# Optimization experiments

Hardware: AMD Instinct MI355X
Metric: run time of the kernel (lower is better)

The kernel has to match this reference:

```python
import jax, jax.numpy as jnp
import numpy as np

B, T, I, U, O, BB = 256, 1024, 64, 256, 64, 128  # batch, seq, input, units, output, backbone_units

def lecun_tanh(x):
    return 1.7159 * jnp.tanh(0.666 * x)

def setup_inputs() -> dict:
    key = jax.random.key(0)
    ks = jax.random.split(key, 13)
    def lin(k, fan_in, fan_out):
        bound = 1.0 / np.sqrt(fan_in)
        kw, kb = jax.random.split(k)
        W = jax.random.uniform(kw, (fan_in, fan_out), jnp.float32, -bound, bound)
        b = jax.random.uniform(kb, (fan_out,), jnp.float32, -bound, bound)
        return W, b
    x = jax.random.normal(ks[0], (B, T, I), jnp.float32)
    W_bb, b_bb = lin(ks[1], I + U, BB)   # backbone Linear
    W_ff1, b_ff1 = lin(ks[2], BB, U)
    W_ff2, b_ff2 = lin(ks[3], BB, U)
    W_ta, b_ta = lin(ks[4], BB, U)       # time_a
    W_tb, b_tb = lin(ks[5], BB, U)       # time_b
    W_fc, b_fc = lin(ks[6], U, O)        # readout
    return {"x": x, "W_bb": W_bb, "b_bb": b_bb, "W_ff1": W_ff1, "b_ff1": b_ff1,
            "W_ff2": W_ff2, "b_ff2": b_ff2, "W_ta": W_ta, "b_ta": b_ta,
            "W_tb": W_tb, "b_tb": b_tb, "W_fc": W_fc, "b_fc": b_fc}

def reference(x, W_bb, b_bb, W_ff1, b_ff1, W_ff2, b_ff2, W_ta, b_ta, W_tb, b_tb, W_fc, b_fc):
    ts = jnp.float32(1.0)  # default elapsed time per step
    def step(h, xt):
        z = jnp.concatenate([xt, h], axis=-1)          # [B, I+U]
        g = lecun_tanh(z @ W_bb + b_bb)                # [B, BB]
        ff1 = jnp.tanh(g @ W_ff1 + b_ff1)              # [B, U]
        ff2 = jnp.tanh(g @ W_ff2 + b_ff2)
        t_interp = jax.nn.sigmoid((g @ W_ta + b_ta) * ts + (g @ W_tb + b_tb))
        h_new = ff1 * (1.0 - t_interp) + t_interp * ff2
        return h_new, h_new
    h0 = jnp.zeros((x.shape[0], U), x.dtype)
    h_last, hs = jax.lax.scan(step, h0, jnp.swapaxes(x, 0, 1))  # hs: [T, B, U]
    hs = jnp.swapaxes(hs, 0, 1)                                  # [B, T, U]
    out = hs @ W_fc + b_fc                                       # [B, T, O]
    return out, h_last
```

## Files before the change

kernel.cpp:

```cpp
#include <hip/hip_runtime.h>
#include <stdint.h>

#define B_ 256
#define T_ 1024
#define I_ 64
#define U_ 256
#define O_ 64
#define BB_ 128

typedef unsigned int u32;
typedef unsigned short u16;
typedef _Float16 half2_t __attribute__((ext_vector_type(2)));

#if defined(__has_builtin)
#if __has_builtin(__builtin_amdgcn_fdot2)
#define USE_DOT2 1
#else
#define USE_DOT2 0
#endif
#else
#define USE_DOT2 0
#endif

static __device__ __forceinline__ u32 packpair(float a, float b) {
  half2_t h; h.x = (_Float16)a; h.y = (_Float16)b;
  return __builtin_bit_cast(u32, h);
}
static __device__ __forceinline__ float unpack_lo(u32 u) {
  half2_t h = __builtin_bit_cast(half2_t, u); return (float)h.x;
}
static __device__ __forceinline__ float unpack_hi(u32 u) {
  half2_t h = __builtin_bit_cast(half2_t, u); return (float)h.y;
}
static __device__ __forceinline__ float dot2acc(u32 w, u32 z, float acc) {
#if USE_DOT2
  return __builtin_amdgcn_fdot2(__builtin_bit_cast(half2_t, w),
                                __builtin_bit_cast(half2_t, z), acc, false);
#else
  half2_t hw = __builtin_bit_cast(half2_t, w);
  half2_t hz = __builtin_bit_cast(half2_t, z);
  acc += (float)hw.x * (float)hz.x;
  acc += (float)hw.y * (float)hz.y;
  return acc;
#endif
}

template <int CTRL>
static __device__ __forceinline__ float dpp_mov_f(float v) {
  return __builtin_bit_cast(float, __builtin_amdgcn_update_dpp(
      0, __builtin_bit_cast(int, v), CTRL, 0xF, 0xF, true));
}
#define DPP_XOR1 0xB1
#define DPP_XOR2 0x4E
#define DPP_HMIR 0x141
#define DPP_MIRR 0x140

static __device__ __forceinline__ float fast_tanh(float x) {
  return 1.0f - 2.0f / (1.0f + __expf(2.0f * x));
}
static __device__ __forceinline__ float fast_sigmoid(float x) {
  return 1.0f / (1.0f + __expf(-x));
}

template <bool DEFER>
__global__ __launch_bounds__(1024)
void cfc_kernel(const float* __restrict__ x,
                const float* __restrict__ W_bb, const float* __restrict__ b_bb,
                const float* __restrict__ W_ff1, const float* __restrict__ b_ff1,
                const float* __restrict__ W_ff2, const float* __restrict__ b_ff2,
                const float* __restrict__ W_ta,  const float* __restrict__ b_ta,
                const float* __restrict__ W_tb,  const float* __restrict__ b_tb,
                const float* __restrict__ W_fc,  const float* __restrict__ b_fc,
                float* __restrict__ out, u32* __restrict__ Hbuf)
{
  __shared__ __align__(16) u32 s_z2[160];
  __shared__ __align__(16) u32 s_g2[64];
  u16* s_gh = (u16*)s_g2;

  const int tid = threadIdx.x;
  const int r   = blockIdx.x;

  const int ca  = tid >> 3;
  const int kga = tid & 7;
  const int jb = tid >> 2;
  const int kq = tid & 3;
  const int ro = tid >> 4;
  const int rk = tid & 15;

  u32 wbb[20];
#pragma unroll
  for (int j = 0; j < 5; ++j)
#pragma unroll
    for (int q = 0; q < 4; ++q) {
      int p = 4 * (kga + 8 * j) + q;
      wbb[4 * j + q] = packpair(W_bb[(2 * p) * BB_ + ca],
                                W_bb[(2 * p + 1) * BB_ + ca]);
    }
  u32 wf1[16], wf2[16], wta[16], wtb[16];
#pragma unroll
  for (int j = 0; j < 4; ++j)
#pragma unroll
    for (int q = 0; q < 4; ++q) {
      int p = 4 * (kq + 4 * j) + q;
      int k0 = 2 * p, k1 = 2 * p + 1;
      wf1[4 * j + q] = packpair(W_ff1[k0 * U_ + jb], W_ff1[k1 * U_ + jb]);
      wf2[4 * j + q] = packpair(W_ff2[k0 * U_ + jb], W_ff2[k1 * U_ + jb]);
      wta[4 * j + q] = packpair(W_ta [k0 * U_ + jb], W_ta [k1 * U_ + jb]);
      wtb[4 * j + q] = packpair(W_tb [k0 * U_ + jb], W_tb [k1 * U_ + jb]);
    }
  u32 wfc[8];
  float bfo = 0.f;
  if (!DEFER) {
#pragma unroll
    for (int j = 0; j < 2; ++j)
#pragma unroll
      for (int q = 0; q < 4; ++q) {
        int p = 4 * (rk + 16 * j) + q;
        wfc[4 * j + q] = packpair(W_fc[(2 * p) * O_ + ro],
                                  W_fc[(2 * p + 1) * O_ + ro]);
      }
    bfo = b_fc[ro];
  }
  const float bbbc = b_bb[ca];
  const float b1 = b_ff1[jb], b2 = b_ff2[jb];
  const float bta = b_ta[jb], btb = b_tb[jb];

  const float* xrow = x + (size_t)r * T_ * I_;
  const size_t out_row = (size_t)r * T_ * O_;
  u32* __restrict__ hrow = DEFER ? (Hbuf + (size_t)r * T_ * (U_ / 2)) : nullptr;

  if (tid < 160) s_z2[tid] = 0u;
  __syncthreads();
  if (tid < 32) {
    float2 xv = ((const float2*)xrow)[tid];
    s_z2[tid] = packpair(xv.x, xv.y);
  }
  __syncthreads();

  for (int t = 0; t < T_; ++t) {
    float2 xv;
    const bool ldx = (tid < 32) && (t + 1 < T_);
    if (ldx) xv = ((const float2*)(xrow + (size_t)(t + 1) * I_))[tid];

    float bacc = 0.f;
#pragma unroll
    for (int j = 0; j < 5; ++j) {
      uint4 zz = *reinterpret_cast<const uint4*>(s_z2 + 4 * (kga + 8 * j));
      bacc = dot2acc(wbb[4 * j + 0], zz.x, bacc);
      bacc = dot2acc(wbb[4 * j + 1], zz.y, bacc);
      bacc = dot2acc(wbb[4 * j + 2], zz.z, bacc);
      bacc = dot2acc(wbb[4 * j + 3], zz.w, bacc);
    }
    bacc += dpp_mov_f<DPP_XOR1>(bacc);
    bacc += dpp_mov_f<DPP_XOR2>(bacc);
    bacc += dpp_mov_f<DPP_HMIR>(bacc);
    float g = 1.7159f * fast_tanh(0.666f * (bacc + bbbc));

    float racc = 0.f;
    if (!DEFER) {
#pragma unroll
      for (int j = 0; j < 2; ++j) {
        uint4 hh = *reinterpret_cast<const uint4*>(s_z2 + 32 + 4 * (rk + 16 * j));
        racc = dot2acc(wfc[4 * j + 0], hh.x, racc);
        racc = dot2acc(wfc[4 * j + 1], hh.y, racc);
        racc = dot2acc(wfc[4 * j + 2], hh.z, racc);
        racc = dot2acc(wfc[4 * j + 3], hh.w, racc);
      }
      racc += dpp_mov_f<DPP_XOR1>(racc);
      racc += dpp_mov_f<DPP_XOR2>(racc);
      racc += dpp_mov_f<DPP_HMIR>(racc);
      racc += dpp_mov_f<DPP_MIRR>(racc);
    }
    if ((tid & 7) == 0)
      s_gh[ca] = __builtin_bit_cast(u16, (_Float16)g);
    if (!DEFER && t > 0 && rk == 0)
      out[out_row + (size_t)(t - 1) * O_ + ro] = racc + bfo;
    __syncthreads();

    float a1 = 0.f, a2 = 0.f, a3 = 0.f, a4 = 0.f;
#pragma unroll
    for (int j = 0; j < 4; ++j) {
      uint4 gg = *reinterpret_cast<const uint4*>(s_g2 + 4 * (kq + 4 * j));
      a1 = dot2acc(wf1[4 * j + 0], gg.x, a1);
      a1 = dot2acc(wf1[4 * j + 1], gg.y, a1);
      a1 = dot2acc(wf1[4 * j + 2], gg.z, a1);
      a1 = dot2acc(wf1[4 * j + 3], gg.w, a1);
      a2 = dot2acc(wf2[4 * j + 0], gg.x, a2);
      a2 = dot2acc(wf2[4 * j + 1], gg.y, a2);
      a2 = dot2acc(wf2[4 * j + 2], gg.z, a2);
      a2 = dot2acc(wf2[4 * j + 3], gg.w, a2);
      a3 = dot2acc(wta[4 * j + 0], gg.x, a3);
      a3 = dot2acc(wta[4 * j + 1], gg.y, a3);
      a3 = dot2acc(wta[4 * j + 2], gg.z, a3);
      a3 = dot2acc(wta[4 * j + 3], gg.w, a3);
      a4 = dot2acc(wtb[4 * j + 0], gg.x, a4);
      a4 = dot2acc(wtb[4 * j + 1], gg.y, a4);
      a4 = dot2acc(wtb[4 * j + 2], gg.z, a4);
      a4 = dot2acc(wtb[4 * j + 3], gg.w, a4);
    }
    a1 += dpp_mov_f<DPP_XOR1>(a1); a1 += dpp_mov_f<DPP_XOR2>(a1);
    a2 += dpp_mov_f<DPP_XOR1>(a2); a2 += dpp_mov_f<DPP_XOR2>(a2);
    a3 += dpp_mov_f<DPP_XOR1>(a3); a3 += dpp_mov_f<DPP_XOR2>(a3);
    a4 += dpp_mov_f<DPP_XOR1>(a4); a4 += dpp_mov_f<DPP_XOR2>(a4);
    float f1 = fast_tanh(a1 + b1);
    float f2 = fast_tanh(a2 + b2);
    float ti = fast_sigmoid(a3 + bta + a4 + btb);
    float h  = f1 + ti * (f2 - f1);
    float hq = dpp_mov_f<DPP_HMIR>(h);

    if ((tid & 7) == 0) {
      u32 pr = packpair(h, hq);
      int m = tid >> 3;
      s_z2[32 + m] = pr;
      if (DEFER) hrow[(size_t)t * (U_ / 2) + m] = pr;
    }
    if (ldx) s_z2[tid] = packpair(xv.x, xv.y);
    __syncthreads();
  }

  if (!DEFER) {
    float racc = 0.f;
#pragma unroll
    for (int j = 0; j < 2; ++j) {
      uint4 hh = *reinterpret_cast<const uint4*>(s_z2 + 32 + 4 * (rk + 16 * j));
      racc = dot2acc(wfc[4 * j + 0], hh.x, racc);
      racc = dot2acc(wfc[4 * j + 1], hh.y, racc);
      racc = dot2acc(wfc[4 * j + 2], hh.z, racc);
      racc = dot2acc(wfc[4 * j + 3], hh.w, racc);
    }
    racc += dpp_mov_f<DPP_XOR1>(racc);
    racc += dpp_mov_f<DPP_XOR2>(racc);
    racc += dpp_mov_f<DPP_HMIR>(racc);
    racc += dpp_mov_f<DPP_MIRR>(racc);
    if (rk == 0)
      out[out_row + (size_t)(T_ - 1) * O_ + ro] = racc + bfo;
  }

  if (tid < 128) {
    u32 hp = s_z2[32 + tid];
    float2 hv; hv.x = unpack_lo(hp); hv.y = unpack_hi(hp);
    ((float2*)(out + (size_t)B_ * T_ * O_))[r * 128 + tid] = hv;
  }
}

__global__ __launch_bounds__(512)
void ro_kernel(const u32* __restrict__ Hbuf,
               const float* __restrict__ W_fc, const float* __restrict__ b_fc,
               float* __restrict__ out)
{
  __shared__ __align__(16) u32 s_h[8 * 128];
  const int tid = threadIdx.x;
  const int o   = tid & 63;
  const int w   = tid >> 6;
  const int r   = blockIdx.x;

  u32 wfc[128];
#pragma unroll
  for (int p = 0; p < 128; ++p)
    wfc[p] = packpair(W_fc[(2 * p) * O_ + o], W_fc[(2 * p + 1) * O_ + o]);
  const float bo = b_fc[o];

  const u32* hrow = Hbuf + (size_t)r * T_ * 128;
  const size_t out_row = (size_t)r * T_ * O_;

  for (int c = 0; c < T_ / 8; ++c) {
    *(uint2*)(s_h + 2 * tid) =
        *(const uint2*)(hrow + (size_t)c * 1024 + 2 * tid);
    __syncthreads();
    float acc = bo;
    const uint4* h4 = reinterpret_cast<const uint4*>(s_h + w * 128);
#pragma unroll
    for (int i = 0; i < 32; ++i) {
      uint4 hh = h4[i];
      acc = dot2acc(wfc[4 * i + 0], hh.x, acc);
      acc = dot2acc(wfc[4 * i + 1], hh.y, acc);
      acc = dot2acc(wfc[4 * i + 2], hh.z, acc);
      acc = dot2acc(wfc[4 * i + 3], hh.w, acc);
    }
    out[out_row + (size_t)(8 * c + w) * O_ + o] = acc;
    __syncthreads();
  }
}

extern "C" void kernel_launch(void* const* d_in, const int* in_sizes, int n_in,
                              void* d_out, int out_size, void* d_ws, size_t ws_size,
                              hipStream_t stream) {
  const float* x     = (const float*)d_in[0];
  const float* W_bb  = (const float*)d_in[1];
  const float* b_bb  = (const float*)d_in[2];
  const float* W_ff1 = (const float*)d_in[3];
  const float* b_ff1 = (const float*)d_in[4];
  const float* W_ff2 = (const float*)d_in[5];
  const float* b_ff2 = (const float*)d_in[6];
  const float* W_ta  = (const float*)d_in[7];
  const float* b_ta  = (const float*)d_in[8];
  const float* W_tb  = (const float*)d_in[9];
  const float* b_tb  = (const float*)d_in[10];
  const float* W_fc  = (const float*)d_in[11];
  const float* b_fc  = (const float*)d_in[12];
  float* out = (float*)d_out;

  const size_t h_bytes = (size_t)B_ * T_ * (U_ / 2) * sizeof(u32);
  if (ws_size >= h_bytes) {
    u32* Hbuf = (u32*)d_ws;
    cfc_kernel<true><<<dim3(B_), dim3(1024), 0, stream>>>(
        x, W_bb, b_bb, W_ff1, b_ff1, W_ff2, b_ff2,
        W_ta, b_ta, W_tb, b_tb, W_fc, b_fc, out, Hbuf);
    ro_kernel<<<dim3(B_), dim3(512), 0, stream>>>(Hbuf, W_fc, b_fc, out);
  } else {
    cfc_kernel<false><<<dim3(B_), dim3(1024), 0, stream>>>(
        x, W_bb, b_bb, W_ff1, b_ff1, W_ff2, b_ff2,
        W_ta, b_ta, W_tb, b_tb, W_fc, b_fc, out, nullptr);
  }
}
```

Baseline: 1.903 ms.

## Compute recurrent step matmuls with MFMA instructions instead of packed dot2

Adds a new recurrence kernel that runs each step's backbone and four gate matmuls with 16x16x32 f16 MFMA instructions. The weights stay in registers as MFMA B fragments, and the backbone is split over K across wave pairs, with partial sums combined through shared memory. Hidden-state writes to the workspace and the prefetch of the next x row are moved onto dedicated waves. The aim is to shorten the serial per-step chain of dot2 and DPP reductions. In exchange it adds a third barrier per step and wastes most MFMA rows, since only one batch row is processed per block.

```diff
diff --git a/kernel.cpp b/kernel.cpp
--- a/kernel.cpp
+++ b/kernel.cpp
@@ -10,6 +10,9 @@
 
 typedef unsigned int u32;
 typedef unsigned short u16;
+typedef _Float16 f16;
+typedef _Float16 f16x8 __attribute__((ext_vector_type(8)));
+typedef float f32x4 __attribute__((ext_vector_type(4)));
 typedef _Float16 half2_t __attribute__((ext_vector_type(2)));
 
 #if defined(__has_builtin)
@@ -23,7 +26,7 @@
 #endif
 
 static __device__ __forceinline__ u32 packpair(float a, float b) {
-  half2_t h; h.x = (_Float16)a; h.y = (_Float16)b;
+  half2_t h; h.x = (f16)a; h.y = (f16)b;
   return __builtin_bit_cast(u32, h);
 }
 static __device__ __forceinline__ float unpack_lo(u32 u) {
@@ -62,16 +65,174 @@
   return 1.0f / (1.0f + __expf(-x));
 }
 
-template <bool DEFER>
+__global__ __launch_bounds__(1024, 4)
+void cfc_mfma_kernel(const float* __restrict__ x,
+                     const float* __restrict__ W_bb, const float* __restrict__ b_bb,
+                     const float* __restrict__ W_ff1, const float* __restrict__ b_ff1,
+                     const float* __restrict__ W_ff2, const float* __restrict__ b_ff2,
+                     const float* __restrict__ W_ta,  const float* __restrict__ b_ta,
+                     const float* __restrict__ W_tb,  const float* __restrict__ b_tb,
+                     float* __restrict__ out, u32* __restrict__ Hbuf)
+{
+  __shared__ __align__(16) f16   s_x[2][64];
+  __shared__ __align__(16) f16   s_h[256];
+  __shared__ __align__(16) f16   s_g[128];
+  __shared__ __align__(16) float s_red[16][16];
+
+  const int tid = threadIdx.x;
+  const int w   = tid >> 6;
+  const int L   = tid & 63;
+  const int l15 = L & 15;
+  const int q   = L >> 4;
+  const int r   = blockIdx.x;
+
+  const int an = w >> 1;
+  const int as = w & 1;
+  f16x8 wbb[5];
+  for (int i = 0; i < 5; ++i) {
+    int kt = 5 * as + i;
+    f16x8 f;
+#pragma unroll
+    for (int j = 0; j < 8; ++j)
+      f[j] = (f16)W_bb[(32 * kt + 8 * q + j) * BB_ + 16 * an + l15];
+    wbb[i] = f;
+  }
+  const int u = 16 * w + l15;
+  const float* Wm[4] = {W_ff1, W_ff2, W_ta, W_tb};
+  f16x8 wf[4][4];
+  for (int m = 0; m < 4; ++m)
+    for (int kt = 0; kt < 4; ++kt) {
+      f16x8 f;
+#pragma unroll
+      for (int j = 0; j < 8; ++j)
+        f[j] = (f16)Wm[m][(32 * kt + 8 * q + j) * U_ + u];
+      wf[m][kt] = f;
+    }
+  const float b1 = b_ff1[u], b2 = b_ff2[u];
+  const float bta = b_ta[u], btb = b_tb[u];
+  float bbbn = 0.f;
+  if (w < 8) bbbn = b_bb[16 * w + l15];
+
+  const float* xrow = x + (size_t)r * T_ * I_;
+  u32* __restrict__ hrow = Hbuf + (size_t)r * T_ * 128;
+
+  if (tid < 128) ((u32*)s_h)[tid] = 0u;
+  if (tid < 32) {
+    float2 xv = ((const float2*)xrow)[tid];
+    half2_t p; p.x = (f16)xv.x; p.y = (f16)xv.y;
+    ((half2_t*)s_x[0])[tid] = p;
+  }
+  __syncthreads();
+
+  for (int t = 0; t < T_; ++t) {
+    const f16* xslot = s_x[t & 1];
+    f32x4 ca = {0.f, 0.f, 0.f, 0.f};
+#pragma unroll
+    for (int i = 0; i < 5; ++i) {
+      int kt = 5 * as + i;
+      const f16* ap = (kt < 2) ? (xslot + 32 * kt + 8 * q)
+                               : (s_h + 32 * (kt - 2) + 8 * q);
+      f16x8 af = *(const f16x8*)ap;
+      ca = __builtin_amdgcn_mfma_f32_16x16x32_f16(af, wbb[i], ca, 0, 0, 0);
+    }
+    if (L < 16) s_red[w][l15] = ca[0];
+    if (w == 8 || w == 9) {
+      if (t > 0) {
+        int idx = (w - 8) * 64 + L;
+        hrow[(size_t)(t - 1) * 128 + idx] = ((const u32*)s_h)[idx];
+      }
+    } else if (w == 10) {
+      if (t + 1 < T_ && L < 32) {
+        float2 xv = ((const float2*)(xrow + (size_t)(t + 1) * I_))[L];
+        half2_t p; p.x = (f16)xv.x; p.y = (f16)xv.y;
+        ((half2_t*)s_x[(t + 1) & 1])[L] = p;
+      }
+    }
+    __syncthreads();
+
+    if (w < 8 && L < 16) {
+      float pre = s_red[2 * w][l15] + s_red[2 * w + 1][l15] + bbbn;
+      s_g[16 * w + l15] = (f16)(1.7159f * fast_tanh(0.666f * pre));
+    }
+    __syncthreads();
+
+    f32x4 c0 = {0,0,0,0}, c1 = {0,0,0,0}, c2 = {0,0,0,0}, c3 = {0,0,0,0};
+#pragma unroll
+    for (int kt = 0; kt < 4; ++kt) {
+      f16x8 gf = *(const f16x8*)(s_g + 32 * kt + 8 * q);
+      c0 = __builtin_amdgcn_mfma_f32_16x16x32_f16(gf, wf[0][kt], c0, 0, 0, 0);
+      c1 = __builtin_amdgcn_mfma_f32_16x16x32_f16(gf, wf[1][kt], c1, 0, 0, 0);
+      c2 = __builtin_amdgcn_mfma_f32_16x16x32_f16(gf, wf[2][kt], c2, 0, 0, 0);
+      c3 = __builtin_amdgcn_mfma_f32_16x16x32_f16(gf, wf[3][kt], c3, 0, 0, 0);
+    }
+    float f1 = fast_tanh(c0[0] + b1);
+    float f2 = fast_tanh(c1[0] + b2);
+    float ti = fast_sigmoid(c2[0] + bta + c3[0] + btb);
+    float h  = f1 + ti * (f2 - f1);
+    float hx = dpp_mov_f<DPP_XOR1>(h);
+    if (L < 16 && !(L & 1)) {
+      half2_t p; p.x = (f16)h; p.y = (f16)hx;
+      ((half2_t*)s_h)[8 * w + (l15 >> 1)] = p;
+    }
+    __syncthreads();
+  }
+
+  if (tid < 128) {
+    u32 hp = ((const u32*)s_h)[tid];
+    hrow[(size_t)(T_ - 1) * 128 + tid] = hp;
+    float2 hv; hv.x = unpack_lo(hp); hv.y = unpack_hi(hp);
+    ((float2*)(out + (size_t)B_ * T_ * O_))[r * 128 + tid] = hv;
+  }
+}
+
+__global__ __launch_bounds__(512)
+void ro_kernel(const u32* __restrict__ Hbuf,
+               const float* __restrict__ W_fc, const float* __restrict__ b_fc,
+               float* __restrict__ out)
+{
+  __shared__ __align__(16) u32 s_hb[8 * 128];
+  const int tid = threadIdx.x;
+  const int o   = tid & 63;
+  const int w   = tid >> 6;
+  const int r   = blockIdx.x;
+
+  u32 wfc[128];
+#pragma unroll
+  for (int p = 0; p < 128; ++p)
+    wfc[p] = packpair(W_fc[(2 * p) * O_ + o], W_fc[(2 * p + 1) * O_ + o]);
+  const float bo = b_fc[o];
+
+  const u32* hrow = Hbuf + (size_t)r * T_ * 128;
+  const size_t out_row = (size_t)r * T_ * O_;
+
+  for (int c = 0; c < T_ / 8; ++c) {
+    *(uint2*)(s_hb + 2 * tid) =
+        *(const uint2*)(hrow + (size_t)c * 1024 + 2 * tid);
+    __syncthreads();
+    float acc = bo;
+    const uint4* h4 = reinterpret_cast<const uint4*>(s_hb + w * 128);
+#pragma unroll
+    for (int i = 0; i < 32; ++i) {
+      uint4 hh = h4[i];
+      acc = dot2acc(wfc[4 * i + 0], hh.x, acc);
+      acc = dot2acc(wfc[4 * i + 1], hh.y, acc);
+      acc = dot2acc(wfc[4 * i + 2], hh.z, acc);
+      acc = dot2acc(wfc[4 * i + 3], hh.w, acc);
+    }
+    out[out_row + (size_t)(8 * c + w) * O_ + o] = acc;
+    __syncthreads();
+  }
+}
+
 __global__ __launch_bounds__(1024)
-void cfc_kernel(const float* __restrict__ x,
+void cfc_dot2_kernel(const float* __restrict__ x,
                 const float* __restrict__ W_bb, const float* __restrict__ b_bb,
                 const float* __restrict__ W_ff1, const float* __restrict__ b_ff1,
                 const float* __restrict__ W_ff2, const float* __restrict__ b_ff2,
                 const float* __restrict__ W_ta,  const float* __restrict__ b_ta,
                 const float* __restrict__ W_tb,  const float* __restrict__ b_tb,
                 const float* __restrict__ W_fc,  const float* __restrict__ b_fc,
-                float* __restrict__ out, u32* __restrict__ Hbuf)
+                float* __restrict__ out)
 {
   __shared__ __align__(16) u32 s_z2[160];
   __shared__ __align__(16) u32 s_g2[64];
@@ -79,7 +240,6 @@
 
   const int tid = threadIdx.x;
   const int r   = blockIdx.x;
-
   const int ca  = tid >> 3;
   const int kga = tid & 7;
   const int jb = tid >> 2;
@@ -91,43 +251,39 @@
 #pragma unroll
   for (int j = 0; j < 5; ++j)
 #pragma unroll
-    for (int q = 0; q < 4; ++q) {
-      int p = 4 * (kga + 8 * j) + q;
-      wbb[4 * j + q] = packpair(W_bb[(2 * p) * BB_ + ca],
-                                W_bb[(2 * p + 1) * BB_ + ca]);
+    for (int qq = 0; qq < 4; ++qq) {
+      int p = 4 * (kga + 8 * j) + qq;
+      wbb[4 * j + qq] = packpair(W_bb[(2 * p) * BB_ + ca],
+                                 W_bb[(2 * p + 1) * BB_ + ca]);
     }
   u32 wf1[16], wf2[16], wta[16], wtb[16];
 #pragma unroll
   for (int j = 0; j < 4; ++j)
 #pragma unroll
-    for (int q = 0; q < 4; ++q) {
-      int p = 4 * (kq + 4 * j) + q;
+    for (int qq = 0; qq < 4; ++qq) {
+      int p = 4 * (kq + 4 * j) + qq;
       int k0 = 2 * p, k1 = 2 * p + 1;
-      wf1[4 * j + q] = packpair(W_ff1[k0 * U_ + jb], W_ff1[k1 * U_ + jb]);
-      wf2[4 * j + q] = packpair(W_ff2[k0 * U_ + jb], W_ff2[k1 * U_ + jb]);
-      wta[4 * j + q] = packpair(W_ta [k0 * U_ + jb], W_ta [k1 * U_ + jb]);
-      wtb[4 * j + q] = packpair(W_tb [k0 * U_ + jb], W_tb [k1 * U_ + jb]);
+      wf1[4 * j + qq] = packpair(W_ff1[k0 * U_ + jb], W_ff1[k1 * U_ + jb]);
+      wf2[4 * j + qq] = packpair(W_ff2[k0 * U_ + jb], W_ff2[k1 * U_ + jb]);
+      wta[4 * j + qq] = packpair(W_ta [k0 * U_ + jb], W_ta [k1 * U_ + jb]);
+      wtb[4 * j + qq] = packpair(W_tb [k0 * U_ + jb], W_tb [k1 * U_ + jb]);
     }
   u32 wfc[8];
-  float bfo = 0.f;
-  if (!DEFER) {
-#pragma unroll
-    for (int j = 0; j < 2; ++j)
-#pragma unroll
-      for (int q = 0; q < 4; ++q) {
-        int p = 4 * (rk + 16 * j) + q;
-        wfc[4 * j + q] = packpair(W_fc[(2 * p) * O_ + ro],
-                                  W_fc[(2 * p + 1) * O_ + ro]);
-      }
-    bfo = b_fc[ro];
-  }
+#pragma unroll
+  for (int j = 0; j < 2; ++j)
+#pragma unroll
+    for (int qq = 0; qq < 4; ++qq) {
+      int p = 4 * (rk + 16 * j) + qq;
+      wfc[4 * j + qq] = packpair(W_fc[(2 * p) * O_ + ro],
+                                 W_fc[(2 * p + 1) * O_ + ro]);
+    }
+  const float bfo = b_fc[ro];
   const float bbbc = b_bb[ca];
   const float b1 = b_ff1[jb], b2 = b_ff2[jb];
   const float bta = b_ta[jb], btb = b_tb[jb];
 
   const float* xrow = x + (size_t)r * T_ * I_;
   const size_t out_row = (size_t)r * T_ * O_;
-  u32* __restrict__ hrow = DEFER ? (Hbuf + (size_t)r * T_ * (U_ / 2)) : nullptr;
 
   if (tid < 160) s_z2[tid] = 0u;
   __syncthreads();
@@ -157,23 +313,22 @@
     float g = 1.7159f * fast_tanh(0.666f * (bacc + bbbc));
 
     float racc = 0.f;
-    if (!DEFER) {
-#pragma unroll
-      for (int j = 0; j < 2; ++j) {
-        uint4 hh = *reinterpret_cast<const uint4*>(s_z2 + 32 + 4 * (rk + 16 * j));
-        racc = dot2acc(wfc[4 * j + 0], hh.x, racc);
-        racc = dot2acc(wfc[4 * j + 1], hh.y, racc);
-        racc = dot2acc(wfc[4 * j + 2], hh.z, racc);
-        racc = dot2acc(wfc[4 * j + 3], hh.w, racc);
-      }
-      racc += dpp_mov_f<DPP_XOR1>(racc);
-      racc += dpp_mov_f<DPP_XOR2>(racc);
-      racc += dpp_mov_f<DPP_HMIR>(racc);
-      racc += dpp_mov_f<DPP_MIRR>(racc);
-    }
+#pragma unroll
+    for (int j = 0; j < 2; ++j) {
+      uint4 hh = *reinterpret_cast<const uint4*>(s_z2 + 32 + 4 * (rk + 16 * j));
+      racc = dot2acc(wfc[4 * j + 0], hh.x, racc);
+      racc = dot2acc(wfc[4 * j + 1], hh.y, racc);
+      racc = dot2acc(wfc[4 * j + 2], hh.z, racc);
+      racc = dot2acc(wfc[4 * j + 3], hh.w, racc);
+    }
+    racc += dpp_mov_f<DPP_XOR1>(racc);
+    racc += dpp_mov_f<DPP_XOR2>(racc);
+    racc += dpp_mov_f<DPP_HMIR>(racc);
+    racc += dpp_mov_f<DPP_MIRR>(racc);
+
     if ((tid & 7) == 0)
-      s_gh[ca] = __builtin_bit_cast(u16, (_Float16)g);
-    if (!DEFER && t > 0 && rk == 0)
+      s_gh[ca] = __builtin_bit_cast(u16, (f16)g);
+    if (t > 0 && rk == 0)
       out[out_row + (size_t)(t - 1) * O_ + ro] = racc + bfo;
     __syncthreads();
 
@@ -208,17 +363,13 @@
     float h  = f1 + ti * (f2 - f1);
     float hq = dpp_mov_f<DPP_HMIR>(h);
 
-    if ((tid & 7) == 0) {
-      u32 pr = packpair(h, hq);
-      int m = tid >> 3;
-      s_z2[32 + m] = pr;
-      if (DEFER) hrow[(size_t)t * (U_ / 2) + m] = pr;
-    }
+    if ((tid & 7) == 0)
+      s_z2[32 + (tid >> 3)] = packpair(h, hq);
     if (ldx) s_z2[tid] = packpair(xv.x, xv.y);
     __syncthreads();
   }
 
-  if (!DEFER) {
+  {
     float racc = 0.f;
 #pragma unroll
     for (int j = 0; j < 2; ++j) {
@@ -240,45 +391,6 @@
     u32 hp = s_z2[32 + tid];
     float2 hv; hv.x = unpack_lo(hp); hv.y = unpack_hi(hp);
     ((float2*)(out + (size_t)B_ * T_ * O_))[r * 128 + tid] = hv;
-  }
-}
-
-__global__ __launch_bounds__(512)
-void ro_kernel(const u32* __restrict__ Hbuf,
-               const float* __restrict__ W_fc, const float* __restrict__ b_fc,
-               float* __restrict__ out)
-{
-  __shared__ __align__(16) u32 s_h[8 * 128];
-  const int tid = threadIdx.x;
-  const int o   = tid & 63;
-  const int w   = tid >> 6;
-  const int r   = blockIdx.x;
-
-  u32 wfc[128];
-#pragma unroll
-  for (int p = 0; p < 128; ++p)
-    wfc[p] = packpair(W_fc[(2 * p) * O_ + o], W_fc[(2 * p + 1) * O_ + o]);
-  const float bo = b_fc[o];
-
-  const u32* hrow = Hbuf + (size_t)r * T_ * 128;
-  const size_t out_row = (size_t)r * T_ * O_;
-
-  for (int c = 0; c < T_ / 8; ++c) {
-    *(uint2*)(s_h + 2 * tid) =
-        *(const uint2*)(hrow + (size_t)c * 1024 + 2 * tid);
-    __syncthreads();
-    float acc = bo;
-    const uint4* h4 = reinterpret_cast<const uint4*>(s_h + w * 128);
-#pragma unroll
-    for (int i = 0; i < 32; ++i) {
-      uint4 hh = h4[i];
-      acc = dot2acc(wfc[4 * i + 0], hh.x, acc);
-      acc = dot2acc(wfc[4 * i + 1], hh.y, acc);
-      acc = dot2acc(wfc[4 * i + 2], hh.z, acc);
-      acc = dot2acc(wfc[4 * i + 3], hh.w, acc);
-    }
-    out[out_row + (size_t)(8 * c + w) * O_ + o] = acc;
-    __syncthreads();
   }
 }
 
@@ -300,16 +412,16 @@
   const float* b_fc  = (const float*)d_in[12];
   float* out = (float*)d_out;
 
-  const size_t h_bytes = (size_t)B_ * T_ * (U_ / 2) * sizeof(u32);
+  const size_t h_bytes = (size_t)B_ * T_ * 128 * sizeof(u32);
   if (ws_size >= h_bytes) {
     u32* Hbuf = (u32*)d_ws;
-    cfc_kernel<true><<<dim3(B_), dim3(1024), 0, stream>>>(
+    cfc_mfma_kernel<<<dim3(B_), dim3(1024), 0, stream>>>(
         x, W_bb, b_bb, W_ff1, b_ff1, W_ff2, b_ff2,
-        W_ta, b_ta, W_tb, b_tb, W_fc, b_fc, out, Hbuf);
+        W_ta, b_ta, W_tb, b_tb, out, Hbuf);
     ro_kernel<<<dim3(B_), dim3(512), 0, stream>>>(Hbuf, W_fc, b_fc, out);
   } else {
-    cfc_kernel<false><<<dim3(B_), dim3(1024), 0, stream>>>(
+    cfc_dot2_kernel<<<dim3(B_), dim3(1024), 0, stream>>>(
         x, W_bb, b_bb, W_ff1, b_ff1, W_ff2, b_ff2,
-        W_ta, b_ta, W_tb, b_tb, W_fc, b_fc, out, nullptr);
-  }
-}
+        W_ta, b_ta, W_tb, b_tb, W_fc, b_fc, out);
+  }
+}
```

After: 2.148 ms. +12.9%, slower.
